# Kernel optimization log

Hardware: AMD Instinct MI355X
Metric: run time of the kernel (lower is better)

Reference implementation:

```python
import jax, jax.numpy as jnp
import numpy as np

B, S, D, H = 2, 2048, 1024, 16
DK = D // H

def setup_inputs() -> dict:
    key = jax.random.key(0)
    ks = jax.random.split(key, 12)
    scale = 1.0 / np.sqrt(D)
    inp = {
        'q': jax.random.normal(ks[0], (B, S, D), jnp.float32),
        'k': jax.random.normal(ks[1], (B, S, D), jnp.float32),
        'v': jax.random.normal(ks[2], (B, S, D), jnp.float32),
        # causal mask: 1 where attending is allowed (j <= i), 0 for future tokens
        'mask': jnp.tril(jnp.ones((S, S), jnp.int32))[None, None, :, :],
        'wq': jax.random.normal(ks[3], (D, D), jnp.float32) * scale,
        'bq': jnp.zeros((D,), jnp.float32),
        'wk': jax.random.normal(ks[4], (D, D), jnp.float32) * scale,
        'bk': jnp.zeros((D,), jnp.float32),
        'wv': jax.random.normal(ks[5], (D, D), jnp.float32) * scale,
        'bv': jnp.zeros((D,), jnp.float32),
        'wo': jax.random.normal(ks[6], (D, D), jnp.float32) * scale,
        'bo': jnp.zeros((D,), jnp.float32),
    }
    return inp


def reference(q, k, v, mask, wq, bq, wk, bk, wv, bv, wo, bo):
    def split_heads(x):
        # [B,S,D] -> [B,H,S,DK]
        return x.reshape(B, S, H, DK).transpose(0, 2, 1, 3)

    query = split_heads(q @ wq + bq)
    key_ = split_heads(k @ wk + bk)
    value = split_heads(v @ wv + bv)

    # [B,H,S,S] attention scores
    scores = jnp.einsum('bhqd,bhkd->bhqk', query, key_) / jnp.sqrt(
        jnp.asarray(DK, jnp.float32))
    scores = jnp.where(mask == 0, jnp.asarray(-1e9, scores.dtype), scores)
    attn = jax.nn.softmax(scores, axis=-1)  # dropout p=0.0 (eval mode)

    x = jnp.einsum('bhqk,bhkd->bhqd', attn, value)  # [B,H,S,DK]
    x = x.transpose(0, 2, 1, 3).reshape(B, S, D)
    return x @ wo + bo
```

## Files before the change

### kernel.cpp

```cpp
#include <hip/hip_runtime.h>
#include <hip/hip_bf16.h>

#define BATCH 2
#define SEQ   2048
#define DMODEL 1024
#define NHEAD 16
#define DK    64
#define MTOK  (BATCH * SEQ)

typedef __attribute__((ext_vector_type(8))) short bf16x8;
typedef __attribute__((ext_vector_type(4))) float f32x4;

__device__ __forceinline__ unsigned short f2bf(float x) {
    unsigned u = __float_as_uint(x);
    u = (u + 0x7FFFu + ((u >> 16) & 1u)) >> 16;
    return (unsigned short)u;
}

__device__ __forceinline__ void store_out(float* p, float v)          { *p = v; }
__device__ __forceinline__ void store_out(unsigned short* p, float v) { *p = f2bf(v); }

__device__ __forceinline__ unsigned cvt_pk_bf16(float x, float y) {
    unsigned d;
    asm("v_cvt_pk_bf16_f32 %0, %1, %2" : "=v"(d) : "v"(x), "v"(y));
    return d;
}

__device__ __forceinline__ void g2lds16(const void* g, void* l) {
    __builtin_amdgcn_global_load_lds(
        (const __attribute__((address_space(1))) void*)g,
        (__attribute__((address_space(3))) void*)l, 16, 0, 0);
}

template <int N>
__device__ __forceinline__ void s_wait_vmcnt() {
    asm volatile("s_waitcnt vmcnt(%0)" :: "n"(N) : "memory");
}
__device__ __forceinline__ void s_wait_lgkm0() {
    asm volatile("s_waitcnt lgkmcnt(0)" ::: "memory");
}
__device__ __forceinline__ void s_bar() {
    asm volatile("s_barrier" ::: "memory");
}

__global__ __launch_bounds__(256) void cvt3_bf16_kernel(
    const float* __restrict__ s0, const float* __restrict__ s1,
    const float* __restrict__ s2,
    unsigned short* __restrict__ d0, unsigned short* __restrict__ d1,
    unsigned short* __restrict__ d2, int n)
{
    const float* src; unsigned short* dst;
    switch (blockIdx.z) {
        case 0:  src = s0; dst = d0; break;
        case 1:  src = s1; dst = d1; break;
        default: src = s2; dst = d2; break;
    }
    int i = (blockIdx.x * 256 + threadIdx.x) * 8;
    if (i >= n) return;
    float4 a = *(const float4*)(src + i);
    float4 b = *(const float4*)(src + i + 4);
    union { unsigned short s[8]; uint4 u; } o;
    o.s[0] = f2bf(a.x); o.s[1] = f2bf(a.y); o.s[2] = f2bf(a.z); o.s[3] = f2bf(a.w);
    o.s[4] = f2bf(b.x); o.s[5] = f2bf(b.y); o.s[6] = f2bf(b.z); o.s[7] = f2bf(b.w);
    *(uint4*)(dst + i) = o.u;
}

__global__ __launch_bounds__(256) void wtrans_kernel(
    const float* __restrict__ w0, const float* __restrict__ w1,
    const float* __restrict__ w2, const float* __restrict__ w3,
    unsigned short* __restrict__ t0, unsigned short* __restrict__ t1,
    unsigned short* __restrict__ t2, unsigned short* __restrict__ t3)
{
    __shared__ float tile[32][33];
    const float* W; unsigned short* T;
    switch (blockIdx.z) {
        case 0:  W = w0; T = t0; break;
        case 1:  W = w1; T = t1; break;
        case 2:  W = w2; T = t2; break;
        default: W = w3; T = t3; break;
    }
    const int n0 = blockIdx.x * 32, k0 = blockIdx.y * 32;
    const int t  = threadIdx.x;
    const int r  = t >> 3;
    const int c4 = (t & 7) * 4;

    float4 v = *(const float4*)&W[(size_t)(k0 + r) * DMODEL + n0 + c4];
    tile[r][c4 + 0] = v.x; tile[r][c4 + 1] = v.y;
    tile[r][c4 + 2] = v.z; tile[r][c4 + 3] = v.w;
    __syncthreads();

    union { unsigned short s[4]; uint2 u; } o;
#pragma unroll
    for (int u = 0; u < 4; ++u) o.s[u] = f2bf(tile[c4 + u][r]);
    *(uint2*)&T[(size_t)(n0 + r) * DMODEL + k0 + c4] = o.u;
}

struct GemmP {
    const unsigned short* A;
    const unsigned short* Bt;
    const float* bias;
    void* C;
    int N, K, ctShift, biasByRow;
    float scale;
};
struct Gemm3 { GemmP p[3]; };

template <typename OutT, int MR, int NC>
__global__ __launch_bounds__(512, 2) void gemm_lds_kernel(Gemm3 g)
{
    constexpr int AM    = MR / 2;
    constexpr int NCW   = NC / 4;
    constexpr int NBLK  = 2 * MR + 2 * NC;
    constexpr int PW    = NBLK / 8;
    constexpr int BUFSZ = NBLK * 512;

    __shared__ unsigned short sS[2 * BUFSZ];

    const unsigned nx  = gridDim.x;
    const unsigned lin = blockIdx.x + nx * blockIdx.z;
    const unsigned ch  = (nx * gridDim.z) >> 3;
    const unsigned l2  = (lin & 7u) * ch + (lin >> 3);
    const unsigned zz  = l2 / nx;
    const unsigned bid = l2 - zz * nx;

    const GemmP p = g.p[zz];
    const unsigned short* __restrict__ A  = p.A;
    const unsigned short* __restrict__ Bt = p.Bt;
    OutT* __restrict__ C = (OutT*)p.C;
    const int K = p.K, N = p.N;

    const int bx = (int)(bid & ((1u << p.ctShift) - 1u));
    const int by = (int)(bid >> p.ctShift);
    const int row0 = by * (MR * 16);
    const int col0 = bx * (NC * 16);

    const int t    = threadIdx.x;
    const int w    = t >> 6;
    const int lane = t & 63;
    const int ln   = lane & 15;
    const int qg   = lane >> 4;
    const int wm   = w >> 2;
    const int wn   = w & 3;

    const unsigned short* sp[PW];
    int lo[PW];
#pragma unroll
    for (int i = 0; i < PW; ++i) {
        const int s = w * PW + i;
        if (s < 2 * MR) {
            const int mtg = s >> 1, kc = s & 1;
            sp[i] = A + (size_t)(row0 + mtg * 16 + ln) * K + kc * 32 + qg * 8;
        } else {
            const int bi = s - 2 * MR;
            const int ntg = bi >> 1, kc = bi & 1;
            sp[i] = Bt + (size_t)(col0 + ntg * 16 + ln) * K + kc * 32 + qg * 8;
        }
        lo[i] = s * 512;
    }

    f32x4 acc[AM][NCW];
#pragma unroll
    for (int mt = 0; mt < AM; ++mt)
#pragma unroll
        for (int nt = 0; nt < NCW; ++nt) acc[mt][nt] = (f32x4){0.f, 0.f, 0.f, 0.f};

    const int NT = K / 64;

#pragma unroll
    for (int i = 0; i < PW; ++i) g2lds16(sp[i], &sS[lo[i]]);
#pragma unroll
    for (int i = 0; i < PW; ++i) g2lds16(sp[i] + 64, &sS[BUFSZ + lo[i]]);

    int curOff = 0;
    for (int kt = 0; kt < NT; ++kt) {
        if (kt < NT - 1) s_wait_vmcnt<PW>();
        else             s_wait_vmcnt<0>();
        s_bar();

        const unsigned short* bufA = &sS[curOff];
        const unsigned short* bufB = &sS[curOff + 2 * MR * 512];
#pragma unroll
        for (int kc = 0; kc < 2; ++kc) {
            bf16x8 aF[AM], bF[NCW];
#pragma unroll
            for (int mt = 0; mt < AM; ++mt)
                aF[mt] = *(const bf16x8*)&bufA[(((wm * AM + mt) * 2) + kc) * 512 + lane * 8];
#pragma unroll
            for (int n2 = 0; n2 < NCW; ++n2)
                bF[n2] = *(const bf16x8*)&bufB[(((wn * NCW + n2) * 2) + kc) * 512 + lane * 8];
#pragma unroll
            for (int mt = 0; mt < AM; ++mt)
#pragma unroll
                for (int n2 = 0; n2 < NCW; ++n2)
                    acc[mt][n2] = __builtin_amdgcn_mfma_f32_16x16x32_bf16(
                        aF[mt], bF[n2], acc[mt][n2], 0, 0, 0);
        }

        s_wait_lgkm0();
        s_bar();

        if (kt + 2 < NT) {
            const int koff = (kt + 2) * 64;
#pragma unroll
            for (int i = 0; i < PW; ++i)
                g2lds16(sp[i] + koff, &sS[curOff + lo[i]]);
        }
        curOff ^= BUFSZ;
    }

    float bcol[NCW], brow[AM][4];
    if (!p.biasByRow) {
#pragma unroll
        for (int n2 = 0; n2 < NCW; ++n2)
            bcol[n2] = p.bias[col0 + (wn * NCW + n2) * 16 + ln];
    } else {
#pragma unroll
        for (int mt = 0; mt < AM; ++mt)
#pragma unroll
            for (int r = 0; r < 4; ++r)
                brow[mt][r] = p.bias[row0 + wm * (AM * 16) + mt * 16 + qg * 4 + r];
    }

#pragma unroll
    for (int mt = 0; mt < AM; ++mt)
#pragma unroll
        for (int n2 = 0; n2 < NCW; ++n2)
#pragma unroll
            for (int r = 0; r < 4; ++r) {
                int row = row0 + wm * (AM * 16) + mt * 16 + qg * 4 + r;
                int col = col0 + (wn * NCW + n2) * 16 + ln;
                float bb = p.biasByRow ? brow[mt][r] : bcol[n2];
                store_out(&C[(size_t)row * N + col], (acc[mt][n2][r] + bb) * p.scale);
            }
}

#define BR 64
#define BC 64

__global__ __launch_bounds__(256) void attn_mfma_kernel(
    const unsigned short* __restrict__ Qg, const unsigned short* __restrict__ Kg,
    const unsigned short* __restrict__ VT, unsigned short* __restrict__ O)
{
    __shared__ unsigned short sK[2][8 * 512];
    __shared__ unsigned short sV[2][8 * 512];
    __shared__ unsigned short sQ[8 * 512];

    const int t    = threadIdx.x;
    const int w    = t >> 6;
    const int lane = t & 63;
    const int ln   = lane & 15;
    const int qg   = lane >> 4;

    const int id  = blockIdx.x;
    const int bh  = id & 31;
    const int qt  = (SEQ / BR - 1) - (id >> 5);
    const int b   = bh >> 4;
    const int h   = bh & 15;
    const int qi0 = qt * BR;

    const size_t rowbase = (size_t)b * SEQ;
    const size_t colbase = (size_t)h * DK;

#pragma unroll
    for (int i = 0; i < 2; ++i) {
        const int s = w * 2 + i;
        const int nt = s >> 1, kc = s & 1;
        g2lds16(Qg + (rowbase + qi0 + w * 16 + ln) * DMODEL + colbase + i * 32 + qg * 8,
                &sQ[s * 512]);
        g2lds16(Kg + (rowbase + nt * 16 + ln) * DMODEL + colbase + kc * 32 + qg * 8,
                &sK[0][s * 512]);
        g2lds16(VT + (size_t)(colbase + nt * 16 + ln) * MTOK + rowbase + kc * 32 + qg * 8,
                &sV[0][s * 512]);
    }
    __syncthreads();

    bf16x8 aq[2];
#pragma unroll
    for (int kc = 0; kc < 2; ++kc)
        aq[kc] = *(const bf16x8*)&sQ[(w * 2 + kc) * 512 + lane * 8];

    f32x4 ofrag[4];
#pragma unroll
    for (int nt = 0; nt < 4; ++nt) ofrag[nt] = (f32x4){0.f, 0.f, 0.f, 0.f};
    float osum_p = 0.f;
    float m_run  = -3.0e38f;

    const int laneA = ((2 * qg) & 3) * 16 + ln;
    const int laneB = ((2 * qg + 1) & 3) * 16 + ln;
    const bool hiSel = (qg >> 1) & 1;

    const int ntiles = qt + 1;
    for (int jt = 0; jt < ntiles; ++jt) {
        const int cur = jt & 1;

        if (jt + 1 < ntiles) {
            const int j1 = (jt + 1) * BC;
            const int nb = cur ^ 1;
#pragma unroll
            for (int i = 0; i < 2; ++i) {
                const int s = w * 2 + i;
                const int nt = s >> 1, kc = s & 1;
                g2lds16(Kg + (rowbase + j1 + nt * 16 + ln) * DMODEL + colbase + kc * 32 + qg * 8,
                        &sK[nb][s * 512]);
                g2lds16(VT + (size_t)(colbase + nt * 16 + ln) * MTOK + rowbase + j1 + kc * 32 + qg * 8,
                        &sV[nb][s * 512]);
            }
        }

        f32x4 sf[4];
#pragma unroll
        for (int nt = 0; nt < 4; ++nt) {
            f32x4 a2 = (f32x4){0.f, 0.f, 0.f, 0.f};
#pragma unroll
            for (int kc = 0; kc < 2; ++kc) {
                bf16x8 bk = *(const bf16x8*)&sK[cur][(nt * 2 + kc) * 512 + lane * 8];
                a2 = __builtin_amdgcn_mfma_f32_16x16x32_bf16(bk, aq[kc], a2, 0, 0, 0);
            }
            sf[nt] = a2;
        }

        if (jt == ntiles - 1) {
            const int qloc = w * 16 + ln;
#pragma unroll
            for (int nt = 0; nt < 4; ++nt)
#pragma unroll
                for (int r = 0; r < 4; ++r)
                    if (nt * 16 + qg * 4 + r > qloc) sf[nt][r] = -1.0e30f;
        }

        float pmax = sf[0][0];
#pragma unroll
        for (int nt = 0; nt < 4; ++nt)
#pragma unroll
            for (int r = 0; r < 4; ++r) pmax = fmaxf(pmax, sf[nt][r]);
        pmax = fmaxf(pmax, __shfl_xor(pmax, 16));
        pmax = fmaxf(pmax, __shfl_xor(pmax, 32));

        const float mn = fmaxf(m_run, pmax);
        const float al = exp2f(m_run - mn);
        m_run = mn;

        float pv[4][4];
        float lsum = 0.f;
#pragma unroll
        for (int nt = 0; nt < 4; ++nt)
#pragma unroll
            for (int r = 0; r < 4; ++r) {
                float e = exp2f(sf[nt][r] - mn);
                pv[nt][r] = e;
                lsum += e;
            }
        osum_p = osum_p * al + lsum;

        float alr[4];
#pragma unroll
        for (int r = 0; r < 4; ++r) alr[r] = __shfl(al, qg * 4 + r);
#pragma unroll
        for (int nt = 0; nt < 4; ++nt)
#pragma unroll
            for (int r = 0; r < 4; ++r) ofrag[nt][r] *= alr[r];

        unsigned pk0[2], pk1[2], pk2[2], pk3[2];
#pragma unroll
        for (int rr = 0; rr < 2; ++rr) {
            pk0[rr] = cvt_pk_bf16(pv[0][2 * rr], pv[0][2 * rr + 1]);
            pk1[rr] = cvt_pk_bf16(pv[1][2 * rr], pv[1][2 * rr + 1]);
            pk2[rr] = cvt_pk_bf16(pv[2][2 * rr], pv[2][2 * rr + 1]);
            pk3[rr] = cvt_pk_bf16(pv[3][2 * rr], pv[3][2 * rr + 1]);
        }
        union { bf16x8 v; unsigned u[4]; } ap[2];
        {
            unsigned s0, s1;
            s0 = (unsigned)__shfl((int)pk0[0], laneA); s1 = (unsigned)__shfl((int)pk1[0], laneA);
            ap[0].u[0] = hiSel ? s1 : s0;
            s0 = (unsigned)__shfl((int)pk0[1], laneA); s1 = (unsigned)__shfl((int)pk1[1], laneA);
            ap[0].u[1] = hiSel ? s1 : s0;
            s0 = (unsigned)__shfl((int)pk0[0], laneB); s1 = (unsigned)__shfl((int)pk1[0], laneB);
            ap[0].u[2] = hiSel ? s1 : s0;
            s0 = (unsigned)__shfl((int)pk0[1], laneB); s1 = (unsigned)__shfl((int)pk1[1], laneB);
            ap[0].u[3] = hiSel ? s1 : s0;
            s0 = (unsigned)__shfl((int)pk2[0], laneA); s1 = (unsigned)__shfl((int)pk3[0], laneA);
            ap[1].u[0] = hiSel ? s1 : s0;
            s0 = (unsigned)__shfl((int)pk2[1], laneA); s1 = (unsigned)__shfl((int)pk3[1], laneA);
            ap[1].u[1] = hiSel ? s1 : s0;
            s0 = (unsigned)__shfl((int)pk2[0], laneB); s1 = (unsigned)__shfl((int)pk3[0], laneB);
            ap[1].u[2] = hiSel ? s1 : s0;
            s0 = (unsigned)__shfl((int)pk2[1], laneB); s1 = (unsigned)__shfl((int)pk3[1], laneB);
            ap[1].u[3] = hiSel ? s1 : s0;
        }

#pragma unroll
        for (int nt = 0; nt < 4; ++nt) {
#pragma unroll
            for (int kc = 0; kc < 2; ++kc) {
                bf16x8 bv = *(const bf16x8*)&sV[cur][(nt * 2 + kc) * 512 + lane * 8];
                ofrag[nt] = __builtin_amdgcn_mfma_f32_16x16x32_bf16(ap[kc].v, bv, ofrag[nt], 0, 0, 0);
            }
        }

        __syncthreads();
    }

    float osum = osum_p + __shfl_xor(osum_p, 16);
    osum += __shfl_xor(osum, 32);
    const float invq = 1.0f / osum;
    float inv[4];
#pragma unroll
    for (int r = 0; r < 4; ++r) inv[r] = __shfl(invq, qg * 4 + r);
#pragma unroll
    for (int nt = 0; nt < 4; ++nt)
#pragma unroll
        for (int r = 0; r < 4; ++r) {
            int gq = qi0 + w * 16 + qg * 4 + r;
            O[(rowbase + gq) * DMODEL + colbase + nt * 16 + ln] =
                f2bf(ofrag[nt][r] * inv[r]);
        }
}

extern "C" void kernel_launch(void* const* d_in, const int* in_sizes, int n_in,
                              void* d_out, int out_size, void* d_ws, size_t ws_size,
                              hipStream_t stream)
{
    const float* q  = (const float*)d_in[0];
    const float* k  = (const float*)d_in[1];
    const float* v  = (const float*)d_in[2];
    const float* wq = (const float*)d_in[4];
    const float* bq = (const float*)d_in[5];
    const float* wk = (const float*)d_in[6];
    const float* bk = (const float*)d_in[7];
    const float* wv = (const float*)d_in[8];
    const float* bv = (const float*)d_in[9];
    const float* wo = (const float*)d_in[10];
    const float* bo = (const float*)d_in[11];
    float* out = (float*)d_out;

    const size_t mat  = (size_t)MTOK * DMODEL;
    const size_t wmat = (size_t)DMODEL * DMODEL;
    unsigned short* Abq = (unsigned short*)d_ws;
    unsigned short* Abk = Abq + mat;
    unsigned short* Abv = Abk + mat;
    unsigned short* WtQ = Abv + mat;
    unsigned short* WtK = WtQ + wmat;
    unsigned short* WtV = WtK + wmat;
    unsigned short* WtO = WtV + wmat;
    unsigned short* Qb  = WtO + wmat;
    unsigned short* Kb  = Qb + mat;
    unsigned short* VT  = Kb + mat;
    unsigned short* CTX = VT + mat;

    cvt3_bf16_kernel<<<dim3((unsigned)(mat / 2048), 1, 3), 256, 0, stream>>>(
        q, k, v, Abq, Abk, Abv, (int)mat);
    wtrans_kernel<<<dim3(32, 32, 4), 256, 0, stream>>>(wq, wk, wv, wo, WtQ, WtK, WtV, WtO);

    const float qscale = 0.125f * 1.44269504088896f;
    Gemm3 g;
    g.p[0] = (GemmP){Abq, WtQ, bq, (void*)Qb, DMODEL, DMODEL, 2, 0, qscale};
    g.p[1] = (GemmP){Abk, WtK, bk, (void*)Kb, DMODEL, DMODEL, 2, 0, 1.0f};
    g.p[2] = (GemmP){WtV, Abv, bv, (void*)VT, MTOK,   DMODEL, 4, 1, 1.0f};
    gemm_lds_kernel<unsigned short, 16, 16><<<dim3(64, 1, 3), 512, 0, stream>>>(g);

    attn_mfma_kernel<<<BATCH * NHEAD * (SEQ / BR), 256, 0, stream>>>(Qb, Kb, VT, CTX);

    Gemm3 go;
    go.p[0] = (GemmP){CTX, WtO, bo, (void*)out, DMODEL, DMODEL, 3, 0, 1.0f};
    go.p[1] = go.p[0];
    go.p[2] = go.p[0];
    gemm_lds_kernel<float, 8, 8><<<dim3(256, 1, 1), 512, 0, stream>>>(go);
}
```

Measured before the change: 257.1 us.

## Split-K output projection with atomics and merge conversion kernels

Merges the activation bf16 conversion and the weight transpose into one launch. Splits the output-projection GEMM's K dimension in two, doubling its grid to 512 blocks so more CUs are occupied. Partial sums are combined with float atomicAdd into an output that is zeroed by a memset, and only the first split adds the bias. The change adds an extra memset pass and atomic traffic, and the floating-point summation order is no longer fixed.

```diff
diff --git a/kernel.cpp b/kernel.cpp
--- a/kernel.cpp
+++ b/kernel.cpp
@@ -43,56 +43,57 @@
     asm volatile("s_barrier" ::: "memory");
 }
 
-__global__ __launch_bounds__(256) void cvt3_bf16_kernel(
-    const float* __restrict__ s0, const float* __restrict__ s1,
-    const float* __restrict__ s2,
-    unsigned short* __restrict__ d0, unsigned short* __restrict__ d1,
-    unsigned short* __restrict__ d2, int n)
-{
-    const float* src; unsigned short* dst;
-    switch (blockIdx.z) {
-        case 0:  src = s0; dst = d0; break;
-        case 1:  src = s1; dst = d1; break;
-        default: src = s2; dst = d2; break;
-    }
-    int i = (blockIdx.x * 256 + threadIdx.x) * 8;
-    if (i >= n) return;
-    float4 a = *(const float4*)(src + i);
-    float4 b = *(const float4*)(src + i + 4);
-    union { unsigned short s[8]; uint4 u; } o;
-    o.s[0] = f2bf(a.x); o.s[1] = f2bf(a.y); o.s[2] = f2bf(a.z); o.s[3] = f2bf(a.w);
-    o.s[4] = f2bf(b.x); o.s[5] = f2bf(b.y); o.s[6] = f2bf(b.z); o.s[7] = f2bf(b.w);
-    *(uint4*)(dst + i) = o.u;
-}
-
-__global__ __launch_bounds__(256) void wtrans_kernel(
+__global__ __launch_bounds__(256) void cvtw_kernel(
+    const float* __restrict__ q, const float* __restrict__ k,
+    const float* __restrict__ v,
+    unsigned short* __restrict__ dq, unsigned short* __restrict__ dk,
+    unsigned short* __restrict__ dv,
     const float* __restrict__ w0, const float* __restrict__ w1,
     const float* __restrict__ w2, const float* __restrict__ w3,
     unsigned short* __restrict__ t0, unsigned short* __restrict__ t1,
-    unsigned short* __restrict__ t2, unsigned short* __restrict__ t3)
+    unsigned short* __restrict__ t2, unsigned short* __restrict__ t3, int n)
 {
     __shared__ float tile[32][33];
-    const float* W; unsigned short* T;
-    switch (blockIdx.z) {
-        case 0:  W = w0; T = t0; break;
-        case 1:  W = w1; T = t1; break;
-        case 2:  W = w2; T = t2; break;
-        default: W = w3; T = t3; break;
-    }
-    const int n0 = blockIdx.x * 32, k0 = blockIdx.y * 32;
-    const int t  = threadIdx.x;
-    const int r  = t >> 3;
-    const int c4 = (t & 7) * 4;
-
-    float4 v = *(const float4*)&W[(size_t)(k0 + r) * DMODEL + n0 + c4];
-    tile[r][c4 + 0] = v.x; tile[r][c4 + 1] = v.y;
-    tile[r][c4 + 2] = v.z; tile[r][c4 + 3] = v.w;
-    __syncthreads();
-
-    union { unsigned short s[4]; uint2 u; } o;
-#pragma unroll
-    for (int u = 0; u < 4; ++u) o.s[u] = f2bf(tile[c4 + u][r]);
-    *(uint2*)&T[(size_t)(n0 + r) * DMODEL + k0 + c4] = o.u;
+    if (blockIdx.z < 3) {
+        const float* src; unsigned short* dst;
+        switch (blockIdx.z) {
+            case 0:  src = q; dst = dq; break;
+            case 1:  src = k; dst = dk; break;
+            default: src = v; dst = dv; break;
+        }
+        int i = (blockIdx.x * 256 + threadIdx.x) * 8;
+        if (i >= n) return;
+        float4 a = *(const float4*)(src + i);
+        float4 b = *(const float4*)(src + i + 4);
+        union { unsigned short s[8]; uint4 u; } o;
+        o.s[0] = f2bf(a.x); o.s[1] = f2bf(a.y); o.s[2] = f2bf(a.z); o.s[3] = f2bf(a.w);
+        o.s[4] = f2bf(b.x); o.s[5] = f2bf(b.y); o.s[6] = f2bf(b.z); o.s[7] = f2bf(b.w);
+        *(uint4*)(dst + i) = o.u;
+    } else {
+        const int wi = (blockIdx.z - 3) * 2 + (blockIdx.x >> 10);
+        const float* W; unsigned short* T;
+        switch (wi) {
+            case 0:  W = w0; T = t0; break;
+            case 1:  W = w1; T = t1; break;
+            case 2:  W = w2; T = t2; break;
+            default: W = w3; T = t3; break;
+        }
+        const int ti = blockIdx.x & 1023;
+        const int n0 = (ti & 31) * 32, k0 = (ti >> 5) * 32;
+        const int t  = threadIdx.x;
+        const int r  = t >> 3;
+        const int c4 = (t & 7) * 4;
+
+        float4 vv = *(const float4*)&W[(size_t)(k0 + r) * DMODEL + n0 + c4];
+        tile[r][c4 + 0] = vv.x; tile[r][c4 + 1] = vv.y;
+        tile[r][c4 + 2] = vv.z; tile[r][c4 + 3] = vv.w;
+        __syncthreads();
+
+        union { unsigned short s[4]; uint2 u; } o;
+#pragma unroll
+        for (int u = 0; u < 4; ++u) o.s[u] = f2bf(tile[c4 + u][r]);
+        *(uint2*)&T[(size_t)(n0 + r) * DMODEL + k0 + c4] = o.u;
+    }
 }
 
 struct GemmP {
@@ -105,8 +106,8 @@
 };
 struct Gemm3 { GemmP p[3]; };
 
-template <typename OutT, int MR, int NC>
-__global__ __launch_bounds__(512, 2) void gemm_lds_kernel(Gemm3 g)
+template <typename OutT, int MR, int NC, bool SPLITK>
+__device__ __forceinline__ void gemm_body(const Gemm3& g)
 {
     constexpr int AM    = MR / 2;
     constexpr int NCW   = NC / 4;
@@ -121,13 +122,18 @@
     const unsigned ch  = (nx * gridDim.z) >> 3;
     const unsigned l2  = (lin & 7u) * ch + (lin >> 3);
     const unsigned zz  = l2 / nx;
-    const unsigned bid = l2 - zz * nx;
+    const unsigned bid0 = l2 - zz * nx;
 
     const GemmP p = g.p[zz];
     const unsigned short* __restrict__ A  = p.A;
     const unsigned short* __restrict__ Bt = p.Bt;
     OutT* __restrict__ C = (OutT*)p.C;
     const int K = p.K, N = p.N;
+
+    int ks = 0; unsigned bid = bid0;
+    if constexpr (SPLITK) { ks = (int)(bid0 >> 8); bid = bid0 & 255u; }
+    const int kbase = SPLITK ? ks * (K >> 1) : 0;
+    const int KS    = SPLITK ? (K >> 1) : K;
 
     const int bx = (int)(bid & ((1u << p.ctShift) - 1u));
     const int by = (int)(bid >> p.ctShift);
@@ -149,11 +155,11 @@
         const int s = w * PW + i;
         if (s < 2 * MR) {
             const int mtg = s >> 1, kc = s & 1;
-            sp[i] = A + (size_t)(row0 + mtg * 16 + ln) * K + kc * 32 + qg * 8;
+            sp[i] = A + (size_t)(row0 + mtg * 16 + ln) * K + kbase + kc * 32 + qg * 8;
         } else {
             const int bi = s - 2 * MR;
             const int ntg = bi >> 1, kc = bi & 1;
-            sp[i] = Bt + (size_t)(col0 + ntg * 16 + ln) * K + kc * 32 + qg * 8;
+            sp[i] = Bt + (size_t)(col0 + ntg * 16 + ln) * K + kbase + kc * 32 + qg * 8;
         }
         lo[i] = s * 512;
     }
@@ -164,7 +170,7 @@
 #pragma unroll
         for (int nt = 0; nt < NCW; ++nt) acc[mt][nt] = (f32x4){0.f, 0.f, 0.f, 0.f};
 
-    const int NT = K / 64;
+    const int NT = KS / 64;
 
 #pragma unroll
     for (int i = 0; i < PW; ++i) g2lds16(sp[i], &sS[lo[i]]);
@@ -220,6 +226,7 @@
             for (int r = 0; r < 4; ++r)
                 brow[mt][r] = p.bias[row0 + wm * (AM * 16) + mt * 16 + qg * 4 + r];
     }
+    const bool addBias = !SPLITK || (ks == 0);
 
 #pragma unroll
     for (int mt = 0; mt < AM; ++mt)
@@ -230,8 +237,19 @@
                 int row = row0 + wm * (AM * 16) + mt * 16 + qg * 4 + r;
                 int col = col0 + (wn * NCW + n2) * 16 + ln;
                 float bb = p.biasByRow ? brow[mt][r] : bcol[n2];
-                store_out(&C[(size_t)row * N + col], (acc[mt][n2][r] + bb) * p.scale);
+                float vv = (acc[mt][n2][r] + (addBias ? bb : 0.f)) * p.scale;
+                if constexpr (SPLITK) atomicAdd((float*)&C[(size_t)row * N + col], vv);
+                else                  store_out(&C[(size_t)row * N + col], vv);
             }
+}
+
+__global__ __launch_bounds__(512, 2) void gemm_qkv_kernel(Gemm3 g)
+{
+    gemm_body<unsigned short, 16, 16, false>(g);
+}
+__global__ __launch_bounds__(512, 2) void gemm_out_kernel(Gemm3 g)
+{
+    gemm_body<float, 8, 8, true>(g);
 }
 
 #define BR 64
@@ -448,16 +466,17 @@
     unsigned short* VT  = Kb + mat;
     unsigned short* CTX = VT + mat;
 
-    cvt3_bf16_kernel<<<dim3((unsigned)(mat / 2048), 1, 3), 256, 0, stream>>>(
-        q, k, v, Abq, Abk, Abv, (int)mat);
-    wtrans_kernel<<<dim3(32, 32, 4), 256, 0, stream>>>(wq, wk, wv, wo, WtQ, WtK, WtV, WtO);
+    hipMemsetAsync(out, 0, mat * sizeof(float), stream);
+
+    cvtw_kernel<<<dim3(2048, 1, 5), 256, 0, stream>>>(
+        q, k, v, Abq, Abk, Abv, wq, wk, wv, wo, WtQ, WtK, WtV, WtO, (int)mat);
 
     const float qscale = 0.125f * 1.44269504088896f;
     Gemm3 g;
     g.p[0] = (GemmP){Abq, WtQ, bq, (void*)Qb, DMODEL, DMODEL, 2, 0, qscale};
     g.p[1] = (GemmP){Abk, WtK, bk, (void*)Kb, DMODEL, DMODEL, 2, 0, 1.0f};
     g.p[2] = (GemmP){WtV, Abv, bv, (void*)VT, MTOK,   DMODEL, 4, 1, 1.0f};
-    gemm_lds_kernel<unsigned short, 16, 16><<<dim3(64, 1, 3), 512, 0, stream>>>(g);
+    gemm_qkv_kernel<<<dim3(64, 1, 3), 512, 0, stream>>>(g);
 
     attn_mfma_kernel<<<BATCH * NHEAD * (SEQ / BR), 256, 0, stream>>>(Qb, Kb, VT, CTX);
 
@@ -465,5 +484,5 @@
     go.p[0] = (GemmP){CTX, WtO, bo, (void*)out, DMODEL, DMODEL, 3, 0, 1.0f};
     go.p[1] = go.p[0];
     go.p[2] = go.p[0];
-    gemm_lds_kernel<float, 8, 8><<<dim3(256, 1, 1), 512, 0, stream>>>(go);
-}
+    gemm_out_kernel<<<dim3(512, 1, 1), 512, 0, stream>>>(go);
+}
```

Result: slower. 279.7 us (+8.8%).
